# Optimization experiments

Hardware: AMD Instinct MI355X
Metric: run time of the kernel (lower is better)

## Reference

```python
import jax, jax.numpy as jnp
import numpy as np

B, L, C_IN, D, H, DFF, NL, NC, PH = 32, 512, 16, 512, 8, 2048, 3, 10, 128
DH = D // H


def circ_conv1d(x, w):
    # x: [B, C, S] with circular padding 1 on spatial dim, w: [O, C, 3]
    xp = jnp.concatenate([x[..., -1:], x, x[..., :1]], axis=-1)
    return jax.lax.conv_general_dilated(xp, w, (1,), 'VALID',
                                        dimension_numbers=('NCH', 'OIH', 'NCH'))


def positional_embedding(length, d):
    pos = jnp.arange(length, dtype=jnp.float32)[:, None]
    div = jnp.exp(jnp.arange(0, d, 2, dtype=jnp.float32) * (-np.log(10000.0) / d))
    pe = jnp.zeros((length, d), jnp.float32)
    pe = pe.at[:, 0::2].set(jnp.sin(pos * div))
    pe = pe.at[:, 1::2].set(jnp.cos(pos * div))
    return pe


def layer_norm(x, g, b):
    m = jnp.mean(x, -1, keepdims=True)
    v = jnp.var(x, -1, keepdims=True)
    return (x - m) / jnp.sqrt(v + 1e-5) * g + b


def projector(x, stats, conv_w, w0, b0, w1, b1, w2):
    # x: [B, L, C_IN] (channels = seq_len, spatial = enc_in), stats: [B, 1, C_IN]
    y = circ_conv1d(x, conv_w)                     # [B, 1, C_IN]
    y = jnp.concatenate([y, stats], axis=1)        # [B, 2, C_IN]
    y = y.reshape(x.shape[0], -1)                  # [B, 2*C_IN]
    h = jax.nn.relu(y @ w0.T + b0)
    h = jax.nn.relu(h @ w1.T + b1)
    return h @ w2.T                                # no bias on output


def setup_inputs() -> dict:
    key = jax.random.key(0)
    ks = iter(jax.random.split(key, 64))
    rn = lambda shape, s=0.02: jax.random.normal(next(ks), shape, jnp.float32) * s
    inp = {
        'x_enc': jax.random.normal(next(ks), (B, L, C_IN), jnp.float32),
        'x_mark_enc': jnp.ones((B, L), jnp.float32),
        'tok_w': rn((D, C_IN, 3)),
        'Wq': rn((NL, D, D)), 'bq': jnp.zeros((NL, D)),
        'Wk': rn((NL, D, D)), 'bk': jnp.zeros((NL, D)),
        'Wv': rn((NL, D, D)), 'bv': jnp.zeros((NL, D)),
        'Wo': rn((NL, D, D)), 'bo': jnp.zeros((NL, D)),
        'W1': rn((NL, DFF, D)), 'b1': jnp.zeros((NL, DFF)),
        'W2': rn((NL, D, DFF)), 'b2': jnp.zeros((NL, D)),
        'ln1_g': jnp.ones((NL, D)), 'ln1_b': jnp.zeros((NL, D)),
        'ln2_g': jnp.ones((NL, D)), 'ln2_b': jnp.zeros((NL, D)),
        'norm_g': jnp.ones((D,)), 'norm_b': jnp.zeros((D,)),
        'proj_w': rn((NC, D * L)), 'proj_b': jnp.zeros((NC,)),
        'tau_conv_w': rn((1, L, 3)), 'tau_w0': rn((PH, 2 * C_IN)), 'tau_b0': jnp.zeros((PH,)),
        'tau_w1': rn((PH, PH)), 'tau_b1': jnp.zeros((PH,)), 'tau_w2': rn((1, PH)),
        'del_conv_w': rn((1, L, 3)), 'del_w0': rn((PH, 2 * C_IN)), 'del_b0': jnp.zeros((PH,)),
        'del_w1': rn((PH, PH)), 'del_b1': jnp.zeros((PH,)), 'del_w2': rn((L, PH)),
    }
    return inp


def reference(x_enc, x_mark_enc, tok_w,
              Wq, bq, Wk, bk, Wv, bv, Wo, bo,
              W1, b1, W2, b2, ln1_g, ln1_b, ln2_g, ln2_b,
              norm_g, norm_b, proj_w, proj_b,
              tau_conv_w, tau_w0, tau_b0, tau_w1, tau_b1, tau_w2,
              del_conv_w, del_w0, del_b0, del_w1, del_b1, del_w2):
    # De-stationary statistics (detached in the original)
    x_raw = jax.lax.stop_gradient(x_enc)
    mean_enc = jnp.mean(x_raw, 1, keepdims=True)                 # [B,1,C]
    std_enc = jnp.sqrt(jnp.var(x_raw, 1, keepdims=True) + 1e-5)  # [B,1,C]
    tau = jnp.exp(projector(x_raw, std_enc, tau_conv_w, tau_w0, tau_b0,
                            tau_w1, tau_b1, tau_w2))             # [B,1]
    delta = projector(x_raw, mean_enc, del_conv_w, del_w0, del_b0,
                      del_w1, del_b1, del_w2)                    # [B,L]

    # DataEmbedding: circular token conv + sinusoidal positional encoding
    tok = circ_conv1d(jnp.transpose(x_enc, (0, 2, 1)), tok_w)    # [B,D,L]
    x = jnp.transpose(tok, (0, 2, 1)) + positional_embedding(L, D)[None]

    scale = 1.0 / np.sqrt(DH)
    tau4 = tau.reshape(B, 1, 1, 1)
    delta4 = delta[:, None, None, :]
    for i in range(NL):
        q = (x @ Wq[i].T + bq[i]).reshape(B, L, H, DH)
        k = (x @ Wk[i].T + bk[i]).reshape(B, L, H, DH)
        v = (x @ Wv[i].T + bv[i]).reshape(B, L, H, DH)
        scores = jnp.einsum('blhe,bshe->bhls', q, k) * tau4 + delta4
        A = jax.nn.softmax(scale * scores, axis=-1)
        o = jnp.einsum('bhls,bshd->blhd', A, v).reshape(B, L, D)
        o = o @ Wo[i].T + bo[i]
        x = layer_norm(x + o, ln1_g[i], ln1_b[i])
        y = jax.nn.gelu(x @ W1[i].T + b1[i], approximate=False) @ W2[i].T + b2[i]
        x = layer_norm(x + y, ln2_g[i], ln2_b[i])
    x = layer_norm(x, norm_g, norm_b)

    out = jax.nn.gelu(x, approximate=False)
    out = out * x_mark_enc[..., None]
    out = out.reshape(B, -1) @ proj_w.T + proj_b                 # [B, NC]
    return out
```

## Files before the change

### kernel.cpp

```cpp
#include <hip/hip_runtime.h>
#include <hip/hip_bf16.h>
#include <cstdint>

#define DEVINL __device__ __forceinline__

typedef unsigned short u16;
typedef short bf16x8 __attribute__((ext_vector_type(8)));
typedef float f32x4 __attribute__((ext_vector_type(4)));

DEVINL u16 f2b(float f) {
    union { float f; uint32_t u; } x{f};
    uint32_t r = x.u + 0x7fffu + ((x.u >> 16) & 1u);
    return (u16)(r >> 16);
}
DEVINL float b2f(u16 h) {
    union { uint32_t u; float f; } x{(uint32_t)h << 16};
    return x.f;
}
DEVINL float gelu_exact(float v) {
    return 0.5f * v * (1.0f + erff(v * 0.70710678118654752f));
}
DEVINL void gload_lds16(const void* g, void* l) {
    __builtin_amdgcn_global_load_lds(
        (const __attribute__((address_space(1))) void*)(uintptr_t)g,
        (__attribute__((address_space(3))) void*)(uint32_t)(uintptr_t)l,
        16, 0, 0);
}

__global__ void f2b_kernel(const float* __restrict__ in, u16* __restrict__ out, int n) {
    int i = (blockIdx.x * 256 + threadIdx.x) * 8;
    if (i + 8 <= n) {
        float4 a = *(const float4*)(in + i);
        float4 b = *(const float4*)(in + i + 4);
        u16 t[8] = {f2b(a.x), f2b(a.y), f2b(a.z), f2b(a.w),
                    f2b(b.x), f2b(b.y), f2b(b.z), f2b(b.w)};
        *(uint4*)(out + i) = *(const uint4*)t;
    }
}

__global__ void packb_kernel(const float* __restrict__ bq, const float* __restrict__ bk,
                             const float* __restrict__ bv, float* __restrict__ out) {
    int idx = blockIdx.x * 256 + threadIdx.x;
    if (idx >= 3 * 1536) return;
    int i = idx / 1536, j = idx - i * 1536;
    float v = (j < 512) ? bq[i * 512 + j]
            : (j < 1024) ? bk[i * 512 + j - 512]
                         : bv[i * 512 + j - 1024];
    out[idx] = v;
}

__global__ void pe_kernel(float* __restrict__ pet) {
    int l = blockIdx.x, d2 = threadIdx.x;
    float freq = expf(-(float)(2 * d2) * 0.0179889460390f);
    float ang = (float)l * freq;
    pet[l * 512 + 2 * d2]     = sinf(ang);
    pet[l * 512 + 2 * d2 + 1] = cosf(ang);
}

__global__ void stats_kernel(const float* __restrict__ xe, float* __restrict__ mean,
                             float* __restrict__ stdv) {
    int b = blockIdx.x, ln = threadIdx.x;
    int c = ln & 15, part = ln >> 4;
    float s = 0.f, sq = 0.f;
    for (int l = part; l < 512; l += 4) {
        float x = xe[(size_t)b * 8192 + l * 16 + c];
        s += x; sq += x * x;
    }
    s += __shfl_xor(s, 16);  s += __shfl_xor(s, 32);
    sq += __shfl_xor(sq, 16); sq += __shfl_xor(sq, 32);
    if (part == 0) {
        float m = s * (1.0f / 512.0f);
        mean[b * 16 + c] = m;
        stdv[b * 16 + c] = sqrtf(sq * (1.0f / 512.0f) - m * m + 1e-5f);
    }
}

__global__ __launch_bounds__(128)
void proj_kernel(const float* __restrict__ xe, const float* __restrict__ stats,
                 const float* __restrict__ cw, const float* __restrict__ w0,
                 const float* __restrict__ b0, const float* __restrict__ w1,
                 const float* __restrict__ b1, const float* __restrict__ w2,
                 float* __restrict__ outp, int outn, int do_exp) {
    __shared__ float zl[32], h0l[128], h1l[128], red[2];
    int b = blockIdx.x, tid = threadIdx.x;
    {
        int c = tid >> 3, part = tid & 7;
        float acc = 0.f;
        for (int l = part; l < 512; l += 8) {
            const float* xr = xe + (size_t)b * 8192 + l * 16;
            float w0v = cw[l * 3 + 0], w1v = cw[l * 3 + 1], w2v = cw[l * 3 + 2];
            acc += xr[(c + 15) & 15] * w0v + xr[c] * w1v + xr[(c + 1) & 15] * w2v;
        }
        acc += __shfl_xor(acc, 1); acc += __shfl_xor(acc, 2); acc += __shfl_xor(acc, 4);
        if (part == 0) zl[c] = acc;
        if (tid < 16) zl[16 + tid] = stats[b * 16 + tid];
    }
    __syncthreads();
    {
        float acc = b0[tid];
        #pragma unroll
        for (int i = 0; i < 32; ++i) acc += zl[i] * w0[tid * 32 + i];
        h0l[tid] = fmaxf(acc, 0.0f);
    }
    __syncthreads();
    {
        float acc = b1[tid];
        for (int i = 0; i < 128; ++i) acc += h0l[i] * w1[tid * 128 + i];
        h1l[tid] = fmaxf(acc, 0.0f);
    }
    __syncthreads();
    if (outn == 1) {
        float p = h1l[tid] * w2[tid];
        p += __shfl_xor(p, 1);  p += __shfl_xor(p, 2);  p += __shfl_xor(p, 4);
        p += __shfl_xor(p, 8);  p += __shfl_xor(p, 16); p += __shfl_xor(p, 32);
        if ((tid & 63) == 0) red[tid >> 6] = p;
        __syncthreads();
        if (tid == 0) {
            float v = red[0] + red[1];
            outp[b] = do_exp ? expf(v) : v;
        }
    } else {
        for (int l = tid; l < outn; l += 128) {
            float acc = 0.f;
            for (int i = 0; i < 128; ++i) acc += h1l[i] * w2[l * 128 + i];
            outp[(size_t)b * outn + l] = acc;
        }
    }
}

__global__ __launch_bounds__(256)
void tokconv_kernel(const float* __restrict__ xe, const float* __restrict__ tw,
                    const float* __restrict__ pet,
                    float* __restrict__ xf, u16* __restrict__ xb) {
    __shared__ float xs[34][16];
    int lt = blockIdx.x, b = blockIdx.y, tid = threadIdx.x;
    int l0 = lt * 32;
    for (int idx = tid; idx < 34 * 16; idx += 256) {
        int r = idx >> 4, c = idx & 15;
        int gl = (l0 - 1 + r + 512) & 511;
        xs[r][c] = xe[(size_t)b * 8192 + gl * 16 + c];
    }
    __syncthreads();
    for (int dd = tid; dd < 512; dd += 256) {
        float twr[48];
        #pragma unroll
        for (int i = 0; i < 48; ++i) twr[i] = tw[dd * 48 + i];
        for (int l = 0; l < 32; ++l) {
            float acc = 0.f;
            #pragma unroll
            for (int c = 0; c < 16; ++c) {
                acc += xs[l][c]     * twr[c * 3 + 0];
                acc += xs[l + 1][c] * twr[c * 3 + 1];
                acc += xs[l + 2][c] * twr[c * 3 + 2];
            }
            float vv = acc + pet[(size_t)(l0 + l) * 512 + dd];
            size_t idx = ((size_t)b * 512 + l0 + l) * 512 + dd;
            xf[idx] = vv;
            xb[idx] = f2b(vv);
        }
    }
}

template <int ACT, int OBF>
__global__ __launch_bounds__(256)
void gemm_bt(const u16* __restrict__ A, const u16* __restrict__ B,
             const float* __restrict__ bias, void* __restrict__ Cv0,
             u16* __restrict__ Cv1, int M, int N, int K, int Kc) {
    __shared__ u16 smem[3][2][128 * 32];
    const int tid = threadIdx.x, wv = tid >> 6, ln = tid & 63;
    const int nwg = gridDim.x * gridDim.y;
    const int bid = blockIdx.y * gridDim.x + blockIdx.x;
    const int wg  = (bid & 7) * (nwg >> 3) + (bid >> 3);
    const int n0 = (wg % gridDim.x) * 128;
    const int m0 = (wg / gridDim.x) * 128;
    const int kz = blockIdx.z;
    const int wm = (wv >> 1) * 64, wn = (wv & 1) * 64;
    const int lo = ln & 15, hi = ln >> 4;
    f32x4 acc[4][4] = {};
    const int r0 = wv * 16 + (ln >> 2);
    const int sl = ln & 3;
    const int k0 = kz * Kc;

    auto stage = [&](int buf, int kt) {
        #pragma unroll
        for (int c = 0; c < 2; ++c) {
            int row = r0 + c * 64;
            int ssl = sl ^ ((row >> 1) & 3);
            int ldsoff = row * 32 + sl * 8;
            gload_lds16(A + (size_t)(m0 + row) * K + kt + ssl * 8, (char*)smem[buf][0] + ldsoff * 2);
            gload_lds16(B + (size_t)(n0 + row) * K + kt + ssl * 8, (char*)smem[buf][1] + ldsoff * 2);
        }
    };

    const int nt = Kc >> 5;
    stage(0, k0);
    if (nt > 1) stage(1, k0 + 32);
    for (int t = 0; t < nt; ++t) {
        if (t + 1 < nt) { asm volatile("s_waitcnt vmcnt(4)" ::: "memory"); }
        else            { asm volatile("s_waitcnt vmcnt(0)" ::: "memory"); }
        __builtin_amdgcn_s_barrier();
        if (t + 2 < nt) stage((t + 2) % 3, k0 + (t + 2) * 32);
        const u16* As = smem[t % 3][0];
        const u16* Bs = smem[t % 3][1];
        bf16x8 af[4], bfr[4];
        #pragma unroll
        for (int i = 0; i < 4; ++i) {
            int row = wm + i * 16 + lo;
            int slot = hi ^ ((row >> 1) & 3);
            af[i] = *(const bf16x8*)(As + row * 32 + slot * 8);
        }
        #pragma unroll
        for (int j = 0; j < 4; ++j) {
            int row = wn + j * 16 + lo;
            int slot = hi ^ ((row >> 1) & 3);
            bfr[j] = *(const bf16x8*)(Bs + row * 32 + slot * 8);
        }
        #pragma unroll
        for (int i = 0; i < 4; ++i)
            #pragma unroll
            for (int j = 0; j < 4; ++j)
                acc[i][j] = __builtin_amdgcn_mfma_f32_16x16x32_bf16(af[i], bfr[j], acc[i][j], 0, 0, 0);
    }
    __syncthreads();

    const bool second = (kz != 0);
    float* ep = (float*)smem + wv * (16 * 68);
    #pragma unroll
    for (int i = 0; i < 4; ++i) {
        #pragma unroll
        for (int j = 0; j < 4; ++j) {
            int col = n0 + wn + j * 16 + lo;
            float bv = second ? 0.0f : bias[col];
            #pragma unroll
            for (int r = 0; r < 4; ++r) {
                float v = acc[i][j][r] + bv;
                if (ACT == 1 && !second) v = gelu_exact(v);
                ep[(hi * 4 + r) * 68 + j * 16 + lo] = v;
            }
        }
        #pragma unroll
        for (int pp = 0; pp < 4; ++pp) {
            int rl = pp * 4 + hi;
            float4 vv = *(const float4*)(ep + rl * 68 + lo * 4);
            size_t row = (size_t)(m0 + wm + i * 16 + rl);
            int col = n0 + wn + lo * 4;
            if (second) {
                u16 t4[4] = {f2b(vv.x), f2b(vv.y), f2b(vv.z), f2b(vv.w)};
                *(uint2*)(Cv1 + row * N + col) = *(const uint2*)t4;
            } else if (OBF) {
                u16 t4[4] = {f2b(vv.x), f2b(vv.y), f2b(vv.z), f2b(vv.w)};
                *(uint2*)((u16*)Cv0 + row * N + col) = *(const uint2*)t4;
            } else {
                *(float4*)((float*)Cv0 + row * N + col) = vv;
            }
        }
    }
}

__global__ __launch_bounds__(512)
void attn2_kernel(const u16* __restrict__ qkv, const float* __restrict__ tau,
                  const float* __restrict__ delta, u16* __restrict__ o) {
    __shared__ u16 KL[64 * 64];
    __shared__ u16 VT[64 * 72];
    __shared__ u16 PL[8][32 * 64];
    const int tid = threadIdx.x, w = tid >> 6, ln = tid & 63;
    const int lo = ln & 15, hi = ln >> 4;
    const int qh = blockIdx.x, h = blockIdx.y, b = blockIdx.z;
    const size_t qrow0 = (size_t)b * 512;
    const u16* qp = qkv;
    const u16* kp = qkv + 512;
    const u16* vp = qkv + 1024;
    const int hofs = h * 64;
    const float ts = tau[b] * 0.125f;
    u16* Pw = (u16*)PL[w];
    const int q0 = qh * 256 + w * 32;

    bf16x8 qa[2][2];
    #pragma unroll
    for (int i = 0; i < 2; ++i)
        #pragma unroll
        for (int ks = 0; ks < 2; ++ks)
            qa[i][ks] = *(const bf16x8*)(qp + (qrow0 + q0 + i * 16 + lo) * 1536 + hofs + ks * 32 + hi * 8);

    float m_run[2] = {-1e30f, -1e30f};
    float l_run[2] = {0.f, 0.f};
    f32x4 oacc[2][4] = {};

    const int vsl = tid & 7, vsr = tid >> 3;
    uint4 vreg = *(const uint4*)(vp + (qrow0 + vsr) * 1536 + hofs + vsl * 8);

    for (int nt = 0; nt < 8; ++nt) {
        __syncthreads();
        {
            int s = tid >> 3, j = tid & 7;
            int jl = j ^ (s & 7);
            gload_lds16(kp + (qrow0 + nt * 64 + s) * 1536 + hofs + jl * 8,
                        (char*)KL + tid * 16);
        }
        {
            u16 tmp[8]; *(uint4*)tmp = vreg;
            #pragma unroll
            for (int e = 0; e < 8; ++e) {
                int d = vsl * 8 + e;
                int byt = d * 144 + (((vsr >> 3) ^ vsl) << 4) + (vsr & 7) * 2;
                *(u16*)((char*)VT + byt) = tmp[e];
            }
        }
        if (nt < 7)
            vreg = *(const uint4*)(vp + (qrow0 + (nt + 1) * 64 + vsr) * 1536 + hofs + vsl * 8);
        __syncthreads();

        f32x4 sacc[2][4] = {};
        #pragma unroll
        for (int ks = 0; ks < 2; ++ks) {
            #pragma unroll
            for (int jn = 0; jn < 4; ++jn) {
                int s = jn * 16 + lo;
                int phys = (ks * 4 + hi) ^ (s & 7);
                bf16x8 kb = *(const bf16x8*)((const char*)KL + s * 128 + phys * 16);
                #pragma unroll
                for (int i = 0; i < 2; ++i)
                    sacc[i][jn] = __builtin_amdgcn_mfma_f32_16x16x32_bf16(kb, qa[i][ks], sacc[i][jn], 0, 0, 0);
            }
        }
        float tmax[2] = {-1e30f, -1e30f};
        #pragma unroll
        for (int jn = 0; jn < 4; ++jn) {
            float4 dv4 = *(const float4*)(delta + b * 512 + nt * 64 + jn * 16 + hi * 4);
            float dv[4] = {dv4.x, dv4.y, dv4.z, dv4.w};
            #pragma unroll
            for (int i = 0; i < 2; ++i)
                #pragma unroll
                for (int r = 0; r < 4; ++r) {
                    float v = sacc[i][jn][r] * ts + dv[r] * 0.125f;
                    sacc[i][jn][r] = v;
                    tmax[i] = fmaxf(tmax[i], v);
                }
        }
        #pragma unroll
        for (int i = 0; i < 2; ++i) {
            tmax[i] = fmaxf(tmax[i], __shfl_xor(tmax[i], 16));
            tmax[i] = fmaxf(tmax[i], __shfl_xor(tmax[i], 32));
            float mnew = fmaxf(m_run[i], tmax[i]);
            float fac = __expf(m_run[i] - mnew);
            m_run[i] = mnew;
            l_run[i] *= fac;
            #pragma unroll
            for (int jd = 0; jd < 4; ++jd)
                #pragma unroll
                for (int r = 0; r < 4; ++r) oacc[i][jd][r] *= fac;
        }
        #pragma unroll
        for (int i = 0; i < 2; ++i) {
            float ls = 0.f;
            #pragma unroll
            for (int jn = 0; jn < 4; ++jn) {
                float p0 = __expf(sacc[i][jn][0] - m_run[i]);
                float p1 = __expf(sacc[i][jn][1] - m_run[i]);
                float p2 = __expf(sacc[i][jn][2] - m_run[i]);
                float p3 = __expf(sacc[i][jn][3] - m_run[i]);
                ls += (p0 + p1) + (p2 + p3);
                uint2 pk;
                pk.x = (uint32_t)f2b(p0) | ((uint32_t)f2b(p1) << 16);
                pk.y = (uint32_t)f2b(p2) | ((uint32_t)f2b(p3) << 16);
                int q = i * 16 + lo;
                int ls16 = jn * 2 + (hi >> 1);
                int byt = q * 128 + (((ls16 ^ (q & 7)) << 4)) + (hi & 1) * 8;
                *(uint2*)((char*)Pw + byt) = pk;
            }
            ls += __shfl_xor(ls, 16);
            ls += __shfl_xor(ls, 32);
            l_run[i] += ls;
        }
        #pragma unroll
        for (int ks2 = 0; ks2 < 2; ++ks2) {
            bf16x8 pa[2];
            #pragma unroll
            for (int i = 0; i < 2; ++i) {
                int q = i * 16 + lo;
                int phys = (ks2 * 4 + hi) ^ (q & 7);
                pa[i] = *(const bf16x8*)((const char*)Pw + q * 128 + phys * 16);
            }
            #pragma unroll
            for (int jd = 0; jd < 4; ++jd) {
                int d = jd * 16 + lo;
                int cs = (ks2 * 4 + hi) ^ ((d >> 3) & 7);
                bf16x8 vb = *(const bf16x8*)((const char*)VT + d * 144 + cs * 16);
                #pragma unroll
                for (int i = 0; i < 2; ++i)
                    oacc[i][jd] = __builtin_amdgcn_mfma_f32_16x16x32_bf16(vb, pa[i], oacc[i][jd], 0, 0, 0);
            }
        }
    }
    #pragma unroll
    for (int i = 0; i < 2; ++i) {
        float inv = 1.0f / l_run[i];
        #pragma unroll
        for (int jd = 0; jd < 4; ++jd) {
            u16 t4[4];
            #pragma unroll
            for (int r = 0; r < 4; ++r) t4[r] = f2b(oacc[i][jd][r] * inv);
            size_t row = qrow0 + q0 + i * 16 + lo;
            *(uint2*)(o + row * 512 + hofs + jd * 16 + hi * 4) = *(const uint2*)t4;
        }
    }
}

__global__ __launch_bounds__(256)
void ln3_kernel(const float* __restrict__ xin, const float* __restrict__ res0,
                const u16* res1, const float* __restrict__ g,
                const float* __restrict__ bta,
                float* __restrict__ xout, u16* xbf) {
    const int row = blockIdx.x * 4 + (threadIdx.x >> 6);
    const int ln = threadIdx.x & 63;
    const float* xr = xin + (size_t)row * 512;
    const float* rr = res0 + (size_t)row * 512;
    const u16* pr = res1 + (size_t)row * 512;
    float4 a = *(const float4*)(xr + ln * 4);
    float4 c = *(const float4*)(xr + 256 + ln * 4);
    float4 ra = *(const float4*)(rr + ln * 4);
    float4 rc = *(const float4*)(rr + 256 + ln * 4);
    uint2 pa_ = *(const uint2*)(pr + ln * 4);
    uint2 pc_ = *(const uint2*)(pr + 256 + ln * 4);
    const u16* pa16 = (const u16*)&pa_;
    const u16* pc16 = (const u16*)&pc_;
    a.x += ra.x + b2f(pa16[0]); a.y += ra.y + b2f(pa16[1]);
    a.z += ra.z + b2f(pa16[2]); a.w += ra.w + b2f(pa16[3]);
    c.x += rc.x + b2f(pc16[0]); c.y += rc.y + b2f(pc16[1]);
    c.z += rc.z + b2f(pc16[2]); c.w += rc.w + b2f(pc16[3]);
    float s = a.x + a.y + a.z + a.w + c.x + c.y + c.z + c.w;
    float sq = a.x*a.x + a.y*a.y + a.z*a.z + a.w*a.w + c.x*c.x + c.y*c.y + c.z*c.z + c.w*c.w;
    #pragma unroll
    for (int m = 1; m < 64; m <<= 1) { s += __shfl_xor(s, m); sq += __shfl_xor(sq, m); }
    float mean = s * 0.001953125f;
    float var = sq * 0.001953125f - mean * mean;
    float rstd = rsqrtf(var + 1e-5f);
    float4 g0 = *(const float4*)(g + ln * 4);
    float4 g1 = *(const float4*)(g + 256 + ln * 4);
    float4 b0 = *(const float4*)(bta + ln * 4);
    float4 b1 = *(const float4*)(bta + 256 + ln * 4);
    float4 o0, o1;
    o0.x = (a.x - mean) * rstd * g0.x + b0.x;
    o0.y = (a.y - mean) * rstd * g0.y + b0.y;
    o0.z = (a.z - mean) * rstd * g0.z + b0.z;
    o0.w = (a.w - mean) * rstd * g0.w + b0.w;
    o1.x = (c.x - mean) * rstd * g1.x + b1.x;
    o1.y = (c.y - mean) * rstd * g1.y + b1.y;
    o1.z = (c.z - mean) * rstd * g1.z + b1.z;
    o1.w = (c.w - mean) * rstd * g1.w + b1.w;
    *(float4*)(xout + (size_t)row * 512 + ln * 4) = o0;
    *(float4*)(xout + (size_t)row * 512 + 256 + ln * 4) = o1;
    u16 t0[4] = {f2b(o0.x), f2b(o0.y), f2b(o0.z), f2b(o0.w)};
    u16 t1[4] = {f2b(o1.x), f2b(o1.y), f2b(o1.z), f2b(o1.w)};
    *(uint2*)(xbf + (size_t)row * 512 + ln * 4) = *(const uint2*)t0;
    *(uint2*)(xbf + (size_t)row * 512 + 256 + ln * 4) = *(const uint2*)t1;
}

__global__ __launch_bounds__(256)
void lngelu_kernel(const float* __restrict__ xin, const float* __restrict__ g,
                   const float* __restrict__ bta, const float* __restrict__ mark,
                   u16* __restrict__ outb) {
    const int row = blockIdx.x * 4 + (threadIdx.x >> 6);
    const int ln = threadIdx.x & 63;
    const float* xr = xin + (size_t)row * 512;
    float4 a = *(const float4*)(xr + ln * 4);
    float4 c = *(const float4*)(xr + 256 + ln * 4);
    float s = a.x + a.y + a.z + a.w + c.x + c.y + c.z + c.w;
    float sq = a.x*a.x + a.y*a.y + a.z*a.z + a.w*a.w + c.x*c.x + c.y*c.y + c.z*c.z + c.w*c.w;
    #pragma unroll
    for (int m = 1; m < 64; m <<= 1) { s += __shfl_xor(s, m); sq += __shfl_xor(sq, m); }
    float mean = s * 0.001953125f;
    float var = sq * 0.001953125f - mean * mean;
    float rstd = rsqrtf(var + 1e-5f);
    float mk = mark[row];
    float4 g0 = *(const float4*)(g + ln * 4);
    float4 g1 = *(const float4*)(g + 256 + ln * 4);
    float4 b0 = *(const float4*)(bta + ln * 4);
    float4 b1 = *(const float4*)(bta + 256 + ln * 4);
    float v0 = gelu_exact((a.x - mean) * rstd * g0.x + b0.x) * mk;
    float v1 = gelu_exact((a.y - mean) * rstd * g0.y + b0.y) * mk;
    float v2 = gelu_exact((a.z - mean) * rstd * g0.z + b0.z) * mk;
    float v3 = gelu_exact((a.w - mean) * rstd * g0.w + b0.w) * mk;
    float v4 = gelu_exact((c.x - mean) * rstd * g1.x + b1.x) * mk;
    float v5 = gelu_exact((c.y - mean) * rstd * g1.y + b1.y) * mk;
    float v6 = gelu_exact((c.z - mean) * rstd * g1.z + b1.z) * mk;
    float v7 = gelu_exact((c.w - mean) * rstd * g1.w + b1.w) * mk;
    u16 t0[4] = {f2b(v0), f2b(v1), f2b(v2), f2b(v3)};
    u16 t1[4] = {f2b(v4), f2b(v5), f2b(v6), f2b(v7)};
    *(uint2*)(outb + (size_t)row * 512 + ln * 4) = *(const uint2*)t0;
    *(uint2*)(outb + (size_t)row * 512 + 256 + ln * 4) = *(const uint2*)t1;
}

__global__ __launch_bounds__(256)
void fproj_kernel(const u16* __restrict__ gb, const u16* __restrict__ pw,
                  const float* __restrict__ pb, float* __restrict__ out) {
    __shared__ float red[32][4];
    int n = blockIdx.x, ks = blockIdx.y, tid = threadIdx.x;
    float acc[32];
    #pragma unroll
    for (int m = 0; m < 32; ++m) acc[m] = 0.f;
    for (int j = 0; j < 8; ++j) {
        size_t k0 = (size_t)ks * 16384 + j * 2048 + tid * 8;
        bf16x8 w8 = *(const bf16x8*)(pw + (size_t)n * 262144 + k0);
        float wf[8];
        #pragma unroll
        for (int e = 0; e < 8; ++e) wf[e] = b2f((u16)w8[e]);
        #pragma unroll
        for (int m = 0; m < 32; ++m) {
            bf16x8 g8 = *(const bf16x8*)(gb + (size_t)m * 262144 + k0);
            float a = acc[m];
            #pragma unroll
            for (int e = 0; e < 8; ++e) a += b2f((u16)g8[e]) * wf[e];
            acc[m] = a;
        }
    }
    int w = tid >> 6;
    #pragma unroll
    for (int m = 0; m < 32; ++m) {
        float s = acc[m];
        s += __shfl_xor(s, 1);  s += __shfl_xor(s, 2);  s += __shfl_xor(s, 4);
        s += __shfl_xor(s, 8);  s += __shfl_xor(s, 16); s += __shfl_xor(s, 32);
        if ((tid & 63) == 0) red[m][w] = s;
    }
    __syncthreads();
    if (tid < 32) {
        int m = tid;
        float s = red[m][0] + red[m][1] + red[m][2] + red[m][3];
        if (ks == 0) s += pb[n];
        atomicAdd(&out[m * 10 + n], s);
    }
}

extern "C" void kernel_launch(void* const* d_in, const int* in_sizes, int n_in,
                              void* d_out, int out_size, void* d_ws, size_t ws_size,
                              hipStream_t stream) {
    const float* x_enc  = (const float*)d_in[0];
    const float* x_mark = (const float*)d_in[1];
    const float* tok_w  = (const float*)d_in[2];
    const float* Wq = (const float*)d_in[3];   const float* bq = (const float*)d_in[4];
    const float* Wk = (const float*)d_in[5];   const float* bk = (const float*)d_in[6];
    const float* Wv = (const float*)d_in[7];   const float* bv = (const float*)d_in[8];
    const float* Wo = (const float*)d_in[9];   const float* bo = (const float*)d_in[10];
    const float* W1 = (const float*)d_in[11];  const float* b1 = (const float*)d_in[12];
    const float* W2 = (const float*)d_in[13];  const float* b2 = (const float*)d_in[14];
    const float* ln1_g = (const float*)d_in[15]; const float* ln1_b = (const float*)d_in[16];
    const float* ln2_g = (const float*)d_in[17]; const float* ln2_b = (const float*)d_in[18];
    const float* norm_g = (const float*)d_in[19]; const float* norm_b = (const float*)d_in[20];
    const float* proj_w = (const float*)d_in[21]; const float* proj_b = (const float*)d_in[22];
    const float* tau_cw = (const float*)d_in[23];
    const float* tau_w0 = (const float*)d_in[24]; const float* tau_b0 = (const float*)d_in[25];
    const float* tau_w1 = (const float*)d_in[26]; const float* tau_b1 = (const float*)d_in[27];
    const float* tau_w2 = (const float*)d_in[28];
    const float* del_cw = (const float*)d_in[29];
    const float* del_w0 = (const float*)d_in[30]; const float* del_b0 = (const float*)d_in[31];
    const float* del_w1 = (const float*)d_in[32]; const float* del_b1 = (const float*)d_in[33];
    const float* del_w2 = (const float*)d_in[34];
    float* out = (float*)d_out;

    char* ws = (char*)d_ws;
    size_t off = 0;
    auto alloc = [&](size_t bytes) -> void* {
        void* p = ws + off;
        off += (bytes + 255) & ~(size_t)255;
        return p;
    };
    u16* wqkvb = (u16*)alloc((size_t)3 * 786432 * 2);
    u16* wob = (u16*)alloc(786432 * 2);
    u16* w1b = (u16*)alloc(3145728 * 2);
    u16* w2b = (u16*)alloc(3145728 * 2);
    u16* pwb = (u16*)alloc(2621440 * 2);
    float* bqkvb = (float*)alloc(3 * 1536 * 4);
    float* petab = (float*)alloc((size_t)262144 * 4);
    float* meanb = (float*)alloc(512 * 4);
    float* stdb  = (float*)alloc(512 * 4);
    float* taub  = (float*)alloc(32 * 4);
    float* delb  = (float*)alloc(16384 * 4);
    float* xf = (float*)alloc((size_t)8388608 * 4);
    u16*  xb  = (u16*)alloc((size_t)8388608 * 2);
    float* sf = (float*)alloc((size_t)8388608 * 4);
    u16* qkvb = (u16*)alloc((size_t)16384 * 1536 * 2);
    u16* ob   = (u16*)alloc((size_t)8388608 * 2);
    u16* hb   = qkvb;
    u16* gbuf = qkvb;
    u16* p1o  = qkvb;
    u16* p1f  = xb;

    auto cvt = [&](const float* src, u16* dst, int n) {
        f2b_kernel<<<dim3((n + 2047) / 2048), dim3(256), 0, stream>>>(src, dst, n);
    };
    for (int i = 0; i < 3; ++i) {
        cvt(Wq + (size_t)i * 262144, wqkvb + (size_t)i * 786432 + 0,      262144);
        cvt(Wk + (size_t)i * 262144, wqkvb + (size_t)i * 786432 + 262144, 262144);
        cvt(Wv + (size_t)i * 262144, wqkvb + (size_t)i * 786432 + 524288, 262144);
    }
    cvt(Wo, wob, 786432);
    cvt(W1, w1b, 3145728); cvt(W2, w2b, 3145728);
    cvt(proj_w, pwb, 2621440);
    packb_kernel<<<dim3(18), dim3(256), 0, stream>>>(bq, bk, bv, bqkvb);
    pe_kernel<<<dim3(512), dim3(256), 0, stream>>>(petab);

    stats_kernel<<<dim3(32), dim3(64), 0, stream>>>(x_enc, meanb, stdb);
    proj_kernel<<<dim3(32), dim3(128), 0, stream>>>(x_enc, stdb, tau_cw, tau_w0, tau_b0,
                                                    tau_w1, tau_b1, tau_w2, taub, 1, 1);
    proj_kernel<<<dim3(32), dim3(128), 0, stream>>>(x_enc, meanb, del_cw, del_w0, del_b0,
                                                    del_w1, del_b1, del_w2, delb, 512, 0);
    tokconv_kernel<<<dim3(16, 32), dim3(256), 0, stream>>>(x_enc, tok_w, petab, xf, xb);

    for (int i = 0; i < 3; ++i) {
        const u16* wqkv_i = wqkvb + (size_t)i * 786432;
        const u16* wo_i = wob + (size_t)i * 262144;
        const u16* w1_i = w1b + (size_t)i * 1048576;
        const u16* w2_i = w2b + (size_t)i * 1048576;
        gemm_bt<0, 1><<<dim3(12, 128, 1), dim3(256), 0, stream>>>(
            xb, wqkv_i, bqkvb + i * 1536, qkvb, nullptr, 16384, 1536, 512, 512);
        attn2_kernel<<<dim3(2, 8, 32), dim3(512), 0, stream>>>(qkvb, taub, delb, ob);
        gemm_bt<0, 0><<<dim3(4, 128, 2), dim3(256), 0, stream>>>(
            ob, wo_i, bo + i * 512, sf, p1o, 16384, 512, 512, 256);
        ln3_kernel<<<dim3(4096), dim3(256), 0, stream>>>(xf, sf, p1o,
            ln1_g + i * 512, ln1_b + i * 512, xf, xb);
        gemm_bt<1, 1><<<dim3(16, 128, 1), dim3(256), 0, stream>>>(
            xb, w1_i, b1 + i * 2048, hb, nullptr, 16384, 2048, 512, 512);
        gemm_bt<0, 0><<<dim3(4, 128, 2), dim3(256), 0, stream>>>(
            hb, w2_i, b2 + i * 512, sf, p1f, 16384, 512, 2048, 1024);
        ln3_kernel<<<dim3(4096), dim3(256), 0, stream>>>(xf, sf, p1f,
            ln2_g + i * 512, ln2_b + i * 512, xf, xb);
    }

    lngelu_kernel<<<dim3(4096), dim3(256), 0, stream>>>(xf, norm_g, norm_b, x_mark, gbuf);
    hipMemsetAsync(d_out, 0, (size_t)out_size * 4, stream);
    fproj_kernel<<<dim3(10, 16), dim3(256), 0, stream>>>(gbuf, pwb, proj_b, out);
}
```

Baseline: 1.001 ms.

## Add 256x256-tile 8-wave pipelined GEMM for QKV and FFN1 projections

Introduces a new bf16 MFMA GEMM kernel with 256x256 output tiles, 8 waves, K-step 64, XOR-swizzled LDS, and interleaved double-buffered global-to-LDS loads across eight MFMA phases with priority hints. It replaces the 128x128 gemm_bt for the QKV projection and the GELU FFN1 projection. The aim is more reuse per loaded tile and better overlap of memory loads with matrix instructions. In exchange it uses far more LDS and registers per block, which lowers occupancy, and it assumes dimensions divisible by 256 and K divisible by 128.

```diff
diff --git a/kernel.cpp b/kernel.cpp
--- a/kernel.cpp
+++ b/kernel.cpp
@@ -157,6 +157,136 @@
             size_t idx = ((size_t)b * 512 + l0 + l) * 512 + dd;
             xf[idx] = vv;
             xb[idx] = f2b(vv);
+        }
+    }
+}
+
+template <int ACT>
+__global__ __launch_bounds__(512)
+void gemm8p(const u16* __restrict__ A, const u16* __restrict__ B,
+            const float* __restrict__ bias, u16* __restrict__ C,
+            int M, int N, int K) {
+    __shared__ u16 Al[2][256 * 64];
+    __shared__ u16 Bl[2][256 * 64];
+    const int tid = threadIdx.x, wv = tid >> 6, ln = tid & 63;
+    const int lo = ln & 15, hi = ln >> 4;
+    const int gx = gridDim.x;
+    const int nwg = gx * gridDim.y;
+    const int bid = blockIdx.y * gx + blockIdx.x;
+    const int wg  = (bid & 7) * (nwg >> 3) + (bid >> 3);
+    const int n0 = (wg % gx) * 256;
+    const int m0 = (wg / gx) * 256;
+    const int wm0 = (wv >> 2) * 128, wn0 = (wv & 3) * 64;
+    const int srow = wv * 8 + (ln >> 3);
+    const int ssl = ln & 7;
+
+    f32x4 acc[8][4] = {};
+    bf16x8 bfr[2][4];
+
+    auto stageA = [&](int buf, int half, int kt) {
+        #pragma unroll
+        for (int c = 0; c < 2; ++c) {
+            int row = half * 128 + srow + c * 64;
+            gload_lds16(A + (size_t)(m0 + row) * K + kt + (ssl ^ (row & 7)) * 8,
+                        (char*)Al[buf] + row * 128 + ssl * 16);
+        }
+    };
+    auto stageB = [&](int buf, int half, int kt) {
+        #pragma unroll
+        for (int c = 0; c < 2; ++c) {
+            int row = half * 128 + srow + c * 64;
+            gload_lds16(B + (size_t)(n0 + row) * K + kt + (ssl ^ (row & 7)) * 8,
+                        (char*)Bl[buf] + row * 128 + ssl * 16);
+        }
+    };
+
+    stageA(0, 0, 0); stageA(0, 1, 0);
+    stageB(0, 0, 0); stageB(0, 1, 0);
+    stageB(1, 0, 64); stageB(1, 1, 64);
+    asm volatile("s_waitcnt vmcnt(4)" ::: "memory");
+    __builtin_amdgcn_s_barrier();
+
+    const int NT2 = K >> 7;
+    for (int t = 0; t < NT2; ++t) {
+        const bool full = (t < NT2 - 1);
+        const int ktA1 = (2 * t + 1) * 64;
+        const int ktN  = (2 * t + 2) * 64;
+        const int ktB1 = (2 * t + 3) * 64;
+        #pragma unroll
+        for (int p = 0; p < 8; ++p) {
+            const int b = p >> 2, q = p & 3;
+            if (q == 0) {
+                #pragma unroll
+                for (int kk = 0; kk < 2; ++kk)
+                    #pragma unroll
+                    for (int j = 0; j < 4; ++j) {
+                        int row = wn0 + j * 16 + lo;
+                        bfr[kk][j] = *(const bf16x8*)((const char*)Bl[b] + row * 128 +
+                                                      (((kk * 4 + hi) ^ (row & 7)) * 16));
+                    }
+            }
+            bf16x8 af[2][2];
+            #pragma unroll
+            for (int kk = 0; kk < 2; ++kk)
+                #pragma unroll
+                for (int c = 0; c < 2; ++c) {
+                    int row = wm0 + (q * 2 + c) * 16 + lo;
+                    af[kk][c] = *(const bf16x8*)((const char*)Al[b] + row * 128 +
+                                                 (((kk * 4 + hi) ^ (row & 7)) * 16));
+                }
+            switch (p) {
+                case 0: stageA(1, 0, ktA1); break;
+                case 1: stageA(1, 1, ktA1); break;
+                case 2: if (full) stageB(0, 0, ktN); break;
+                case 3: if (full) stageB(0, 1, ktN); break;
+                case 4: if (full) stageA(0, 0, ktN); break;
+                case 5: if (full) stageA(0, 1, ktN); break;
+                case 6: if (full) stageB(1, 0, ktB1); break;
+                case 7: if (full) stageB(1, 1, ktB1); break;
+            }
+            __builtin_amdgcn_sched_barrier(0);
+            __builtin_amdgcn_s_barrier();
+            __builtin_amdgcn_s_setprio(1);
+            #pragma unroll
+            for (int kk = 0; kk < 2; ++kk)
+                #pragma unroll
+                for (int c = 0; c < 2; ++c)
+                    #pragma unroll
+                    for (int j = 0; j < 4; ++j)
+                        acc[q * 2 + c][j] = __builtin_amdgcn_mfma_f32_16x16x32_bf16(
+                            af[kk][c], bfr[kk][j], acc[q * 2 + c][j], 0, 0, 0);
+            __builtin_amdgcn_s_setprio(0);
+            __builtin_amdgcn_sched_barrier(0);
+            if (p == 3 || p == 7) {
+                if (full) { asm volatile("s_waitcnt vmcnt(4)" ::: "memory"); }
+                else      { asm volatile("s_waitcnt vmcnt(0)" ::: "memory"); }
+            }
+            __builtin_amdgcn_s_barrier();
+        }
+    }
+
+    float* ep = (float*)&Al[0][0] + wv * (16 * 68);
+    #pragma unroll
+    for (int i = 0; i < 8; ++i) {
+        #pragma unroll
+        for (int j = 0; j < 4; ++j) {
+            int col = n0 + wn0 + j * 16 + lo;
+            float bv = bias[col];
+            #pragma unroll
+            for (int r = 0; r < 4; ++r) {
+                float v = acc[i][j][r] + bv;
+                if (ACT == 1) v = gelu_exact(v);
+                ep[(hi * 4 + r) * 68 + j * 16 + lo] = v;
+            }
+        }
+        #pragma unroll
+        for (int pp = 0; pp < 4; ++pp) {
+            int rl = pp * 4 + hi;
+            float4 vv = *(const float4*)(ep + rl * 68 + lo * 4);
+            size_t row = (size_t)(m0 + wm0 + i * 16 + rl);
+            int col = n0 + wn0 + lo * 4;
+            u16 t4[4] = {f2b(vv.x), f2b(vv.y), f2b(vv.z), f2b(vv.w)};
+            *(uint2*)(C + row * N + col) = *(const uint2*)t4;
         }
     }
 }
@@ -611,15 +741,15 @@
         const u16* wo_i = wob + (size_t)i * 262144;
         const u16* w1_i = w1b + (size_t)i * 1048576;
         const u16* w2_i = w2b + (size_t)i * 1048576;
-        gemm_bt<0, 1><<<dim3(12, 128, 1), dim3(256), 0, stream>>>(
-            xb, wqkv_i, bqkvb + i * 1536, qkvb, nullptr, 16384, 1536, 512, 512);
+        gemm8p<0><<<dim3(6, 64), dim3(512), 0, stream>>>(
+            xb, wqkv_i, bqkvb + i * 1536, qkvb, 16384, 1536, 512);
         attn2_kernel<<<dim3(2, 8, 32), dim3(512), 0, stream>>>(qkvb, taub, delb, ob);
         gemm_bt<0, 0><<<dim3(4, 128, 2), dim3(256), 0, stream>>>(
             ob, wo_i, bo + i * 512, sf, p1o, 16384, 512, 512, 256);
         ln3_kernel<<<dim3(4096), dim3(256), 0, stream>>>(xf, sf, p1o,
             ln1_g + i * 512, ln1_b + i * 512, xf, xb);
-        gemm_bt<1, 1><<<dim3(16, 128, 1), dim3(256), 0, stream>>>(
-            xb, w1_i, b1 + i * 2048, hb, nullptr, 16384, 2048, 512, 512);
+        gemm8p<1><<<dim3(8, 64), dim3(512), 0, stream>>>(
+            xb, w1_i, b1 + i * 2048, hb, 16384, 2048, 512);
         gemm_bt<0, 0><<<dim3(4, 128, 2), dim3(256), 0, stream>>>(
             hb, w2_i, b2 + i * 512, sf, p1f, 16384, 512, 2048, 1024);
         ln3_kernel<<<dim3(4096), dim3(256), 0, stream>>>(xf, sf, p1f,
```

Result: no change. 982.4 us (-1.9%).
